# Optimization experiments

Measured on AMD Instinct MI355X. Metric: run time of the kernel, lower is better.

## Reference

```python
import jax, jax.numpy as jnp
import numpy as np

D_MODEL = 1024
N_HEADS = 16
D_K = D_MODEL // N_HEADS


def setup_inputs() -> dict:
    key = jax.random.key(0)
    ks = jax.random.split(key, 11)
    B, S = 4, 2048
    scale = 1.0 / np.sqrt(D_MODEL)
    inp = {
        "Q": jax.random.normal(ks[0], (B, S, D_MODEL), jnp.float32),
        "K": jax.random.normal(ks[1], (B, S, D_MODEL), jnp.float32),
        "V": jax.random.normal(ks[2], (B, S, D_MODEL), jnp.float32),
        "Wq": jax.random.normal(ks[3], (D_MODEL, D_MODEL), jnp.float32) * scale,
        "bq": jnp.zeros((D_MODEL,), jnp.float32),
        "Wk": jax.random.normal(ks[4], (D_MODEL, D_MODEL), jnp.float32) * scale,
        "bk": jnp.zeros((D_MODEL,), jnp.float32),
        "Wv": jax.random.normal(ks[5], (D_MODEL, D_MODEL), jnp.float32) * scale,
        "bv": jnp.zeros((D_MODEL,), jnp.float32),
        "Wo": jax.random.normal(ks[6], (D_MODEL, D_MODEL), jnp.float32) * scale,
        "bo": jnp.zeros((D_MODEL,), jnp.float32),
    }
    return inp


def _split_heads(x):
    B, S, _ = x.shape
    return x.reshape(B, S, N_HEADS, D_K).transpose(0, 2, 1, 3)  # [B,H,S,Dk]


def reference(Q, K, V, Wq, bq, Wk, bk, Wv, bv, Wo, bo):
    # torch nn.Linear: y = x @ W.T + b
    q = _split_heads(Q @ Wq.T + bq)
    k = _split_heads(K @ Wk.T + bk)
    v = _split_heads(V @ Wv.T + bv)
    scores = jnp.einsum("bhsd,bhtd->bhst", q, k) / jnp.sqrt(jnp.float32(D_K))
    probs = jax.nn.softmax(scores, axis=-1)
    attn = jnp.einsum("bhst,bhtd->bhsd", probs, v)  # [B,H,S,Dk]
    B, H, S, Dk = attn.shape
    combined = attn.transpose(0, 2, 1, 3).reshape(B, S, H * Dk)
    return combined @ Wo.T + bo
```

## Files before the change

### kernel.cpp

```cpp
#include <hip/hip_runtime.h>
#include <hip/hip_bf16.h>

typedef float  f32x4  __attribute__((ext_vector_type(4)));
typedef float  f32x16 __attribute__((ext_vector_type(16)));
typedef float  fvec4  __attribute__((ext_vector_type(4)));
typedef __bf16 bf16x8 __attribute__((ext_vector_type(8)));
typedef unsigned short u16x4 __attribute__((ext_vector_type(4)));
typedef unsigned short u16x8 __attribute__((ext_vector_type(8)));
typedef unsigned int   u32x4 __attribute__((ext_vector_type(4)));

#define DEVINL __device__ __forceinline__

constexpr int D_MODEL = 1024;
constexpr int NH      = 16;
constexpr int DK      = 64;
constexpr int SEQ     = 2048;
constexpr int BATCH   = 4;
constexpr int M_TOK   = BATCH * SEQ;

DEVINL unsigned short f32_to_bf16_u(float f) {
    unsigned int u = __builtin_bit_cast(unsigned int, f);
    u = (u + 0x7FFFu + ((u >> 16) & 1u)) >> 16;
    return (unsigned short)u;
}

DEVINL float exp2_fast(float x) { return __builtin_amdgcn_exp2f(x); }
DEVINL float mx3(float a, float b, float c) { return fmaxf(fmaxf(a, b), c); }

DEVINL unsigned cvt_pk_bf16(float lo, float hi_) {
    unsigned d;
    asm("v_cvt_pk_bf16_f32 %0, %1, %2" : "=v"(d) : "v"(lo), "v"(hi_));
    return d;
}

DEVINL void gload_lds16(const void* g, void* l) {
    __builtin_amdgcn_global_load_lds(
        (const __attribute__((address_space(1))) void*)g,
        (__attribute__((address_space(3))) void*)l, 16, 0, 0);
}

DEVINL int vperm_s(int s0) { return (s0 & ~12) | ((s0 & 4) << 1) | ((s0 & 8) >> 1); }

__global__ __launch_bounds__(256) void cvt4(const float* __restrict__ a,
                                            const float* __restrict__ b,
                                            const float* __restrict__ c,
                                            const float* __restrict__ d,
                                            unsigned short* __restrict__ dst, int n8)
{
    int y = blockIdx.y;
    const float* s = (y == 0) ? a : (y == 1) ? b : (y == 2) ? c : d;
    size_t i = blockIdx.x * 256 + threadIdx.x;
    fvec4 v0 = *reinterpret_cast<const fvec4*>(s + i * 8);
    fvec4 v1 = *reinterpret_cast<const fvec4*>(s + i * 8 + 4);
    bf16x8 o;
    #pragma unroll
    for (int j = 0; j < 4; ++j) { o[j] = (__bf16)v0[j]; o[j + 4] = (__bf16)v1[j]; }
    *reinterpret_cast<bf16x8*>(dst + ((size_t)y * n8 + i) * 8) = o;
}

__global__ __launch_bounds__(256) void cvt3(const float* __restrict__ a,
                                            const float* __restrict__ b,
                                            const float* __restrict__ c,
                                            unsigned short* __restrict__ dst, int n8)
{
    int y = blockIdx.y;
    const float* s = (y == 0) ? a : (y == 1) ? b : c;
    size_t i = blockIdx.x * 256 + threadIdx.x;
    fvec4 v0 = *reinterpret_cast<const fvec4*>(s + i * 8);
    fvec4 v1 = *reinterpret_cast<const fvec4*>(s + i * 8 + 4);
    bf16x8 o;
    #pragma unroll
    for (int j = 0; j < 4; ++j) { o[j] = (__bf16)v0[j]; o[j + 4] = (__bf16)v1[j]; }
    *reinterpret_cast<bf16x8*>(dst + ((size_t)y * n8 + i) * 8) = o;
}

template<bool QKV>
__global__ __launch_bounds__(256) void gemm_bf(
    const unsigned short* __restrict__ A0, const unsigned short* __restrict__ W0,
    const float* __restrict__ B0, void* __restrict__ O0,
    const unsigned short* __restrict__ A1, const unsigned short* __restrict__ W1,
    const float* __restrict__ B1, void* __restrict__ O1,
    const unsigned short* __restrict__ A2, const unsigned short* __restrict__ W2,
    const float* __restrict__ B2, void* __restrict__ O2,
    float qscale)
{
    constexpr int K = D_MODEL, N = D_MODEL;
    __shared__ char As_[128 * 64 * 2];
    __shared__ char Bs_[128 * 64 * 2];

    const int y = QKV ? (int)blockIdx.y : 0;
    const unsigned short* Ap = (y == 0) ? A0 : (y == 1) ? A1 : A2;
    const unsigned short* Wb = (y == 0) ? W0 : (y == 1) ? W1 : W2;
    const float* bias = (y == 0) ? B0 : (y == 1) ? B1 : B2;

    const int tid  = threadIdx.x;
    const int lane = tid & 63;
    const int wave = tid >> 6;
    const int wr = (wave >> 1) * 64;
    const int wc = (wave & 1) * 64;
    const int wg = ((int)blockIdx.x & 7) * 64 + ((int)blockIdx.x >> 3);
    const int n0 = (wg & 7) * 128;
    const int m0 = (wg >> 3) * 128;
    const int l15 = lane & 15, h16 = lane >> 4;

    f32x4 acc[4][4] = {};

    for (int kt = 0; kt < K; kt += 64) {
        __syncthreads();
        #pragma unroll
        for (int i = 0; i < 4; ++i) {
            int chunk = tid + i * 256;
            int r = chunk >> 3, c16 = chunk & 7;
            int cs = (c16 ^ (r & 7)) * 8;
            gload_lds16(Wb + (size_t)(n0 + r) * K + kt + cs, Bs_ + chunk * 16);
            gload_lds16(Ap + (size_t)(m0 + r) * K + kt + cs, As_ + chunk * 16);
        }
        __syncthreads();

        #pragma unroll
        for (int kk = 0; kk < 2; ++kk) {
            bf16x8 af[4], bfr[4];
            #pragma unroll
            for (int mi = 0; mi < 4; ++mi) {
                int r = wr + mi * 16 + l15;
                af[mi] = *reinterpret_cast<const bf16x8*>(
                    As_ + ((r * 128 + kk * 64 + h16 * 16) ^ ((r & 7) << 4)));
            }
            #pragma unroll
            for (int ni = 0; ni < 4; ++ni) {
                int r = wc + ni * 16 + l15;
                bfr[ni] = *reinterpret_cast<const bf16x8*>(
                    Bs_ + ((r * 128 + kk * 64 + h16 * 16) ^ ((r & 7) << 4)));
            }
            #pragma unroll
            for (int mi = 0; mi < 4; ++mi)
                #pragma unroll
                for (int ni = 0; ni < 4; ++ni)
                    acc[mi][ni] = __builtin_amdgcn_mfma_f32_16x16x32_bf16(
                        af[mi], bfr[ni], acc[mi][ni], 0, 0, 0);
        }
    }

    const int rl = h16 * 4;
    #pragma unroll
    for (int mi = 0; mi < 4; ++mi) {
        #pragma unroll
        for (int ni = 0; ni < 4; ++ni) {
            int col = n0 + wc + ni * 16 + l15;
            float bv = bias[col];
            if constexpr (QKV) {
                float sc = (y == 0) ? qscale : 1.0f;
                if (y == 2) {
                    int row0 = m0 + wr + mi * 16 + rl;
                    int bb = row0 >> 11, s0 = row0 & (SEQ - 1);
                    int sp = vperm_s(s0);
                    int h = col >> 6, dk = col & (DK - 1);
                    u16x4 o;
                    #pragma unroll
                    for (int r = 0; r < 4; ++r)
                        o[r] = f32_to_bf16_u(acc[mi][ni][r] + bv);
                    *reinterpret_cast<u16x4*>((unsigned short*)O2 +
                        (((size_t)bb * NH + h) * DK + dk) * SEQ + sp) = o;
                } else {
                    unsigned short* op = (unsigned short*)((y == 0) ? O0 : O1);
                    #pragma unroll
                    for (int r = 0; r < 4; ++r) {
                        int row = m0 + wr + mi * 16 + rl + r;
                        int bb = row >> 11, s = row & (SEQ - 1);
                        int h = col >> 6, dk = col & (DK - 1);
                        op[((((size_t)bb * NH + h) * SEQ) + s) * DK + dk]
                            = f32_to_bf16_u((acc[mi][ni][r] + bv) * sc);
                    }
                }
            } else {
                #pragma unroll
                for (int r = 0; r < 4; ++r) {
                    int row = m0 + wr + mi * 16 + rl + r;
                    ((float*)O0)[(size_t)row * N + col] = acc[mi][ni][r] + bv;
                }
            }
        }
    }
}

template<int OMODE>
__global__ __launch_bounds__(256) void gemm_f32a(const float* __restrict__ Ap,
                                                 const unsigned short* __restrict__ Wb,
                                                 const float* __restrict__ bias,
                                                 void* __restrict__ outp,
                                                 float out_scale)
{
    constexpr int K = D_MODEL, N = D_MODEL;
    __shared__ char As_[128 * 64 * 2];
    __shared__ char Bs_[128 * 64 * 2];

    const int tid  = threadIdx.x;
    const int lane = tid & 63;
    const int wave = tid >> 6;
    const int wr = (wave >> 1) * 64;
    const int wc = (wave & 1) * 64;
    const int wg = ((int)blockIdx.x & 7) * 64 + ((int)blockIdx.x >> 3);
    const int n0 = (wg & 7) * 128;
    const int m0 = (wg >> 3) * 128;
    const int l15 = lane & 15, h16 = lane >> 4;

    f32x4 acc[4][4] = {};

    for (int kt = 0; kt < K; kt += 64) {
        __syncthreads();
        #pragma unroll
        for (int i = 0; i < 4; ++i) {
            int chunk = tid + i * 256;
            int r = chunk >> 3, c16 = chunk & 7;
            int cs = (c16 ^ (r & 7)) * 8;
            gload_lds16(Wb + (size_t)(n0 + r) * K + kt + cs, Bs_ + chunk * 16);
            const float* src = Ap + (size_t)(m0 + r) * K + kt + c16 * 8;
            fvec4 v0 = *reinterpret_cast<const fvec4*>(src);
            fvec4 v1 = *reinterpret_cast<const fvec4*>(src + 4);
            bf16x8 o;
            #pragma unroll
            for (int j = 0; j < 4; ++j) { o[j] = (__bf16)v0[j]; o[j + 4] = (__bf16)v1[j]; }
            *reinterpret_cast<bf16x8*>(As_ + ((chunk * 16) ^ ((r & 7) << 4))) = o;
        }
        __syncthreads();

        #pragma unroll
        for (int kk = 0; kk < 2; ++kk) {
            bf16x8 af[4], bfr[4];
            #pragma unroll
            for (int mi = 0; mi < 4; ++mi) {
                int r = wr + mi * 16 + l15;
                af[mi] = *reinterpret_cast<const bf16x8*>(
                    As_ + ((r * 128 + kk * 64 + h16 * 16) ^ ((r & 7) << 4)));
            }
            #pragma unroll
            for (int ni = 0; ni < 4; ++ni) {
                int r = wc + ni * 16 + l15;
                bfr[ni] = *reinterpret_cast<const bf16x8*>(
                    Bs_ + ((r * 128 + kk * 64 + h16 * 16) ^ ((r & 7) << 4)));
            }
            #pragma unroll
            for (int mi = 0; mi < 4; ++mi)
                #pragma unroll
                for (int ni = 0; ni < 4; ++ni)
                    acc[mi][ni] = __builtin_amdgcn_mfma_f32_16x16x32_bf16(
                        af[mi], bfr[ni], acc[mi][ni], 0, 0, 0);
        }
    }

    const int rl = h16 * 4;
    #pragma unroll
    for (int mi = 0; mi < 4; ++mi) {
        #pragma unroll
        for (int ni = 0; ni < 4; ++ni) {
            int col = n0 + wc + ni * 16 + l15;
            float bv = bias[col];
            if constexpr (OMODE == 2) {
                int row0 = m0 + wr + mi * 16 + rl;
                int bb = row0 >> 11, s0 = row0 & (SEQ - 1);
                int sp = vperm_s(s0);
                int h = col >> 6, dk = col & (DK - 1);
                u16x4 o;
                #pragma unroll
                for (int r = 0; r < 4; ++r)
                    o[r] = f32_to_bf16_u((acc[mi][ni][r] + bv) * out_scale);
                *reinterpret_cast<u16x4*>((unsigned short*)outp +
                    (((size_t)bb * NH + h) * DK + dk) * SEQ + sp) = o;
            } else {
                #pragma unroll
                for (int r = 0; r < 4; ++r) {
                    int row = m0 + wr + mi * 16 + rl + r;
                    int bb = row >> 11, s = row & (SEQ - 1);
                    int h = col >> 6, dk = col & (DK - 1);
                    ((unsigned short*)outp)[((((size_t)bb * NH + h) * SEQ) + s) * DK + dk]
                        = f32_to_bf16_u((acc[mi][ni][r] + bv) * out_scale);
                }
            }
        }
    }
}

__global__ __launch_bounds__(512, 4) void attn_kernel(const unsigned short* __restrict__ qb,
                                                      const unsigned short* __restrict__ kb,
                                                      const unsigned short* __restrict__ vt,
                                                      unsigned short* __restrict__ ob)
{
    constexpr float THR = 11.0f;
    __shared__ char lds[32768];

    const int tid  = threadIdx.x;
    const int lane = tid & 63;
    const int tl31 = lane & 31;
    const int hi   = lane >> 5;
    const int wave = tid >> 6;
    const int wg   = ((int)blockIdx.x & 7) * 64 + ((int)blockIdx.x >> 3);
    const int bh   = wg >> 3;
    const int q0   = (wg & 7) * 256;
    const size_t base  = (size_t)bh * SEQ * DK;
    const size_t baseT = (size_t)bh * DK * SEQ;

    const int k_kt = tid >> 8, k_kd = (tid >> 6) & 3, k_hi = (tid >> 5) & 1, k_tl = tid & 31;
    const size_t k_goff = base + (size_t)(k_kt * 32 + k_tl) * DK + k_kd * 16 + k_hi * 8;
    const int v_tg = tid >> 6, v_dh = (tid >> 5) & 1, v_dl = tid & 31;
    const size_t v_goff = baseT + (size_t)(v_dh * 32 + v_dl) * SEQ + v_tg * 8;

    bf16x8 qf[4];
    #pragma unroll
    for (int kd = 0; kd < 4; ++kd)
        qf[kd] = *reinterpret_cast<const bf16x8*>(
            qb + base + (size_t)(q0 + wave * 32 + tl31) * DK + kd * 16 + hi * 8);

    f32x16 oaccT[2] = {};
    float m_run = -1e30f, l_run = 0.f;

    {
        u16x8 kreg = *reinterpret_cast<const u16x8*>(kb + k_goff);
        u16x8 vreg = *reinterpret_cast<const u16x8*>(vt + v_goff);
        *reinterpret_cast<u16x8*>(lds + tid * 16) = kreg;
        *reinterpret_cast<u16x8*>(lds + 8192 + tid * 16) = vreg;
    }
    __syncthreads();

    for (int t = 0; t < 32; ++t) {
        const int cur = t & 1;
        const char* Kr = lds + cur * 16384;
        const char* Vr = Kr + 8192;

        u16x8 kreg, vreg;
        if (t < 31) {
            const int t0n = (t + 1) * 64;
            kreg = *reinterpret_cast<const u16x8*>(kb + k_goff + (size_t)t0n * DK);
            vreg = *reinterpret_cast<const u16x8*>(vt + v_goff + t0n);
        }

        f32x16 sT[2] = {};
        #pragma unroll
        for (int kt = 0; kt < 2; ++kt)
            #pragma unroll
            for (int kd = 0; kd < 4; ++kd) {
                bf16x8 kf = *reinterpret_cast<const bf16x8*>(Kr + kt * 4096 + kd * 1024 + lane * 16);
                sT[kt] = __builtin_amdgcn_mfma_f32_32x32x16_bf16(kf, qf[kd], sT[kt], 0, 0, 0);
            }

        float m;
        {
            float tm[2];
            #pragma unroll
            for (int kt = 0; kt < 2; ++kt) {
                float g0 = mx3(sT[kt][0],  sT[kt][1],  sT[kt][2]);
                float g1 = mx3(sT[kt][3],  sT[kt][4],  sT[kt][5]);
                float g2 = mx3(sT[kt][6],  sT[kt][7],  sT[kt][8]);
                float g3 = mx3(sT[kt][9],  sT[kt][10], sT[kt][11]);
                float g4 = mx3(sT[kt][12], sT[kt][13], sT[kt][14]);
                tm[kt] = fmaxf(mx3(g0, g1, g2), mx3(g3, g4, sT[kt][15]));
            }
            m = fmaxf(tm[0], tm[1]);
            m = fmaxf(m, __shfl_xor(m, 32));
        }
        if (__any(m > m_run + THR)) {
            float mn = fmaxf(m_run, m);
            float al = exp2_fast(m_run - mn);
            m_run = mn;
            l_run *= al;
            oaccT[0] *= al;
            oaccT[1] *= al;
        }
        {
            float rs0 = 0.f, rs1 = 0.f, rs2 = 0.f, rs3 = 0.f;
            #pragma unroll
            for (int kt = 0; kt < 2; ++kt)
                #pragma unroll
                for (int i = 0; i < 16; i += 4) {
                    float p0 = exp2_fast(sT[kt][i + 0] - m_run);
                    float p1 = exp2_fast(sT[kt][i + 1] - m_run);
                    float p2 = exp2_fast(sT[kt][i + 2] - m_run);
                    float p3 = exp2_fast(sT[kt][i + 3] - m_run);
                    sT[kt][i + 0] = p0; sT[kt][i + 1] = p1;
                    sT[kt][i + 2] = p2; sT[kt][i + 3] = p3;
                    rs0 += p0; rs1 += p1; rs2 += p2; rs3 += p3;
                }
            float rs = (rs0 + rs1) + (rs2 + rs3);
            rs += __shfl_xor(rs, 32);
            l_run += rs;
        }

        #pragma unroll
        for (int ks = 0; ks < 4; ++ks) {
            bf16x8 vfA0 = *reinterpret_cast<const bf16x8*>(Vr + ks * 2048 + hi * 1024 + tl31 * 16);
            bf16x8 vfA1 = *reinterpret_cast<const bf16x8*>(Vr + ks * 2048 + hi * 1024 + 512 + tl31 * 16);
            const int kt = ks >> 1, r0 = (ks & 1) * 8;
            u32x4 w;
            w[0] = cvt_pk_bf16(sT[kt][r0 + 0], sT[kt][r0 + 1]);
            w[1] = cvt_pk_bf16(sT[kt][r0 + 2], sT[kt][r0 + 3]);
            w[2] = cvt_pk_bf16(sT[kt][r0 + 4], sT[kt][r0 + 5]);
            w[3] = cvt_pk_bf16(sT[kt][r0 + 6], sT[kt][r0 + 7]);
            bf16x8 pa = __builtin_bit_cast(bf16x8, w);
            oaccT[0] = __builtin_amdgcn_mfma_f32_32x32x16_bf16(vfA0, pa, oaccT[0], 0, 0, 0);
            oaccT[1] = __builtin_amdgcn_mfma_f32_32x32x16_bf16(vfA1, pa, oaccT[1], 0, 0, 0);
        }

        if (t < 31) {
            char* Kw = lds + (cur ^ 1) * 16384;
            *reinterpret_cast<u16x8*>(Kw + tid * 16) = kreg;
            *reinterpret_cast<u16x8*>(Kw + 8192 + tid * 16) = vreg;
        }
        __syncthreads();
    }

    char* myregion = lds + wave * 4096;
    const int bb = bh >> 4, h = bh & 15;
    {
        float rl = 1.0f / l_run;
        #pragma unroll
        for (int dh = 0; dh < 2; ++dh)
            #pragma unroll
            for (int r = 0; r < 16; ++r) {
                int dl = (r & 3) + 8 * (r >> 2) + 4 * hi + 32 * dh;
                int boff = (tl31 * 128 + dl * 2) ^ ((tl31 & 7) << 4);
                *reinterpret_cast<unsigned short*>(myregion + boff) =
                    f32_to_bf16_u(oaccT[dh][r] * rl);
            }
        #pragma unroll
        for (int c = 0; c < 4; ++c) {
            int chunk = lane + c * 64;
            int row = chunk >> 3, c16 = chunk & 7;
            int boff = (row * 128 + c16 * 16) ^ ((row & 7) << 4);
            u16x8 v = *reinterpret_cast<const u16x8*>(myregion + boff);
            size_t tok = (size_t)(bb * SEQ) + q0 + wave * 32 + row;
            *reinterpret_cast<u16x8*>(ob + tok * D_MODEL + h * DK + c16 * 8) = v;
        }
    }
}

extern "C" void kernel_launch(void* const* d_in, const int* in_sizes, int n_in,
                              void* d_out, int out_size, void* d_ws, size_t ws_size,
                              hipStream_t stream)
{
    const float* Q  = (const float*)d_in[0];
    const float* K_ = (const float*)d_in[1];
    const float* V  = (const float*)d_in[2];
    const float* Wq = (const float*)d_in[3];
    const float* bq = (const float*)d_in[4];
    const float* Wk = (const float*)d_in[5];
    const float* bk = (const float*)d_in[6];
    const float* Wv = (const float*)d_in[7];
    const float* bv = (const float*)d_in[8];
    const float* Wo = (const float*)d_in[9];
    const float* bo = (const float*)d_in[10];
    float* out = (float*)d_out;

    const size_t SZ = (size_t)M_TOK * D_MODEL;
    const size_t WZ = (size_t)D_MODEL * D_MODEL;
    unsigned short* qh_ = (unsigned short*)d_ws;
    unsigned short* kh_ = qh_ + SZ;
    unsigned short* vh_ = kh_ + SZ;
    unsigned short* ah_ = vh_ + SZ;
    unsigned short* wqb = ah_ + SZ;
    unsigned short* wkb = wqb + WZ;
    unsigned short* wvb = wkb + WZ;
    unsigned short* wob = wvb + WZ;
    unsigned short* qbf = wob + WZ;
    unsigned short* kbf = qbf + SZ;
    unsigned short* vbf = kbf + SZ;

    const bool big = ws_size >= (size_t)(4 * SZ + 4 * WZ + 3 * SZ) * 2;
    const float qscale = 0.125f * 1.4426950408889634f;

    cvt4<<<dim3((int)(WZ / 8 / 256), 4), 256, 0, stream>>>(Wq, Wk, Wv, Wo, wqb, (int)(WZ / 8));

    if (big) {
        cvt3<<<dim3((int)(SZ / 8 / 256), 3), 256, 0, stream>>>(Q, K_, V, qbf, (int)(SZ / 8));
        gemm_bf<true><<<dim3(512, 3), 256, 0, stream>>>(
            qbf, wqb, bq, qh_,  kbf, wkb, bk, kh_,  vbf, wvb, bv, vh_, qscale);
    } else {
        gemm_f32a<1><<<512, 256, 0, stream>>>(Q,  wqb, bq, qh_, qscale);
        gemm_f32a<1><<<512, 256, 0, stream>>>(K_, wkb, bk, kh_, 1.0f);
        gemm_f32a<2><<<512, 256, 0, stream>>>(V,  wvb, bv, vh_, 1.0f);
    }
    attn_kernel<<<512, 512, 0, stream>>>(qh_, kh_, vh_, ah_);
    gemm_bf<false><<<dim3(512, 1), 256, 0, stream>>>(
        ah_, wob, bo, out,  nullptr, nullptr, nullptr, nullptr,
        nullptr, nullptr, nullptr, nullptr, 1.0f);
}
```

Measured before the change: 203.7 us.

## Drop input bf16 pre-conversion path and add MFMA priority hints in attention

Measured after the change: 203.6 us. Within noise of the previous version (-0.1%).

```diff
diff --git a/kernel.cpp b/kernel.cpp
--- a/kernel.cpp
+++ b/kernel.cpp
@@ -58,131 +58,6 @@
     *reinterpret_cast<bf16x8*>(dst + ((size_t)y * n8 + i) * 8) = o;
 }
 
-__global__ __launch_bounds__(256) void cvt3(const float* __restrict__ a,
-                                            const float* __restrict__ b,
-                                            const float* __restrict__ c,
-                                            unsigned short* __restrict__ dst, int n8)
-{
-    int y = blockIdx.y;
-    const float* s = (y == 0) ? a : (y == 1) ? b : c;
-    size_t i = blockIdx.x * 256 + threadIdx.x;
-    fvec4 v0 = *reinterpret_cast<const fvec4*>(s + i * 8);
-    fvec4 v1 = *reinterpret_cast<const fvec4*>(s + i * 8 + 4);
-    bf16x8 o;
-    #pragma unroll
-    for (int j = 0; j < 4; ++j) { o[j] = (__bf16)v0[j]; o[j + 4] = (__bf16)v1[j]; }
-    *reinterpret_cast<bf16x8*>(dst + ((size_t)y * n8 + i) * 8) = o;
-}
-
-template<bool QKV>
-__global__ __launch_bounds__(256) void gemm_bf(
-    const unsigned short* __restrict__ A0, const unsigned short* __restrict__ W0,
-    const float* __restrict__ B0, void* __restrict__ O0,
-    const unsigned short* __restrict__ A1, const unsigned short* __restrict__ W1,
-    const float* __restrict__ B1, void* __restrict__ O1,
-    const unsigned short* __restrict__ A2, const unsigned short* __restrict__ W2,
-    const float* __restrict__ B2, void* __restrict__ O2,
-    float qscale)
-{
-    constexpr int K = D_MODEL, N = D_MODEL;
-    __shared__ char As_[128 * 64 * 2];
-    __shared__ char Bs_[128 * 64 * 2];
-
-    const int y = QKV ? (int)blockIdx.y : 0;
-    const unsigned short* Ap = (y == 0) ? A0 : (y == 1) ? A1 : A2;
-    const unsigned short* Wb = (y == 0) ? W0 : (y == 1) ? W1 : W2;
-    const float* bias = (y == 0) ? B0 : (y == 1) ? B1 : B2;
-
-    const int tid  = threadIdx.x;
-    const int lane = tid & 63;
-    const int wave = tid >> 6;
-    const int wr = (wave >> 1) * 64;
-    const int wc = (wave & 1) * 64;
-    const int wg = ((int)blockIdx.x & 7) * 64 + ((int)blockIdx.x >> 3);
-    const int n0 = (wg & 7) * 128;
-    const int m0 = (wg >> 3) * 128;
-    const int l15 = lane & 15, h16 = lane >> 4;
-
-    f32x4 acc[4][4] = {};
-
-    for (int kt = 0; kt < K; kt += 64) {
-        __syncthreads();
-        #pragma unroll
-        for (int i = 0; i < 4; ++i) {
-            int chunk = tid + i * 256;
-            int r = chunk >> 3, c16 = chunk & 7;
-            int cs = (c16 ^ (r & 7)) * 8;
-            gload_lds16(Wb + (size_t)(n0 + r) * K + kt + cs, Bs_ + chunk * 16);
-            gload_lds16(Ap + (size_t)(m0 + r) * K + kt + cs, As_ + chunk * 16);
-        }
-        __syncthreads();
-
-        #pragma unroll
-        for (int kk = 0; kk < 2; ++kk) {
-            bf16x8 af[4], bfr[4];
-            #pragma unroll
-            for (int mi = 0; mi < 4; ++mi) {
-                int r = wr + mi * 16 + l15;
-                af[mi] = *reinterpret_cast<const bf16x8*>(
-                    As_ + ((r * 128 + kk * 64 + h16 * 16) ^ ((r & 7) << 4)));
-            }
-            #pragma unroll
-            for (int ni = 0; ni < 4; ++ni) {
-                int r = wc + ni * 16 + l15;
-                bfr[ni] = *reinterpret_cast<const bf16x8*>(
-                    Bs_ + ((r * 128 + kk * 64 + h16 * 16) ^ ((r & 7) << 4)));
-            }
-            #pragma unroll
-            for (int mi = 0; mi < 4; ++mi)
-                #pragma unroll
-                for (int ni = 0; ni < 4; ++ni)
-                    acc[mi][ni] = __builtin_amdgcn_mfma_f32_16x16x32_bf16(
-                        af[mi], bfr[ni], acc[mi][ni], 0, 0, 0);
-        }
-    }
-
-    const int rl = h16 * 4;
-    #pragma unroll
-    for (int mi = 0; mi < 4; ++mi) {
-        #pragma unroll
-        for (int ni = 0; ni < 4; ++ni) {
-            int col = n0 + wc + ni * 16 + l15;
-            float bv = bias[col];
-            if constexpr (QKV) {
-                float sc = (y == 0) ? qscale : 1.0f;
-                if (y == 2) {
-                    int row0 = m0 + wr + mi * 16 + rl;
-                    int bb = row0 >> 11, s0 = row0 & (SEQ - 1);
-                    int sp = vperm_s(s0);
-                    int h = col >> 6, dk = col & (DK - 1);
-                    u16x4 o;
-                    #pragma unroll
-                    for (int r = 0; r < 4; ++r)
-                        o[r] = f32_to_bf16_u(acc[mi][ni][r] + bv);
-                    *reinterpret_cast<u16x4*>((unsigned short*)O2 +
-                        (((size_t)bb * NH + h) * DK + dk) * SEQ + sp) = o;
-                } else {
-                    unsigned short* op = (unsigned short*)((y == 0) ? O0 : O1);
-                    #pragma unroll
-                    for (int r = 0; r < 4; ++r) {
-                        int row = m0 + wr + mi * 16 + rl + r;
-                        int bb = row >> 11, s = row & (SEQ - 1);
-                        int h = col >> 6, dk = col & (DK - 1);
-                        op[((((size_t)bb * NH + h) * SEQ) + s) * DK + dk]
-                            = f32_to_bf16_u((acc[mi][ni][r] + bv) * sc);
-                    }
-                }
-            } else {
-                #pragma unroll
-                for (int r = 0; r < 4; ++r) {
-                    int row = m0 + wr + mi * 16 + rl + r;
-                    ((float*)O0)[(size_t)row * N + col] = acc[mi][ni][r] + bv;
-                }
-            }
-        }
-    }
-}
-
 template<int OMODE>
 __global__ __launch_bounds__(256) void gemm_f32a(const float* __restrict__ Ap,
                                                  const unsigned short* __restrict__ Wb,
@@ -190,7 +65,7 @@
                                                  void* __restrict__ outp,
                                                  float out_scale)
 {
-    constexpr int K = D_MODEL, N = D_MODEL;
+    constexpr int K = D_MODEL;
     __shared__ char As_[128 * 64 * 2];
     __shared__ char Bs_[128 * 64 * 2];
 
@@ -280,6 +155,79 @@
     }
 }
 
+__global__ __launch_bounds__(256) void gemm_obf(const unsigned short* __restrict__ Ap,
+                                                const unsigned short* __restrict__ Wb,
+                                                const float* __restrict__ bias,
+                                                float* __restrict__ outp)
+{
+    constexpr int K = D_MODEL, N = D_MODEL;
+    __shared__ char As_[128 * 64 * 2];
+    __shared__ char Bs_[128 * 64 * 2];
+
+    const int tid  = threadIdx.x;
+    const int lane = tid & 63;
+    const int wave = tid >> 6;
+    const int wr = (wave >> 1) * 64;
+    const int wc = (wave & 1) * 64;
+    const int wg = ((int)blockIdx.x & 7) * 64 + ((int)blockIdx.x >> 3);
+    const int n0 = (wg & 7) * 128;
+    const int m0 = (wg >> 3) * 128;
+    const int l15 = lane & 15, h16 = lane >> 4;
+
+    f32x4 acc[4][4] = {};
+
+    for (int kt = 0; kt < K; kt += 64) {
+        __syncthreads();
+        #pragma unroll
+        for (int i = 0; i < 4; ++i) {
+            int chunk = tid + i * 256;
+            int r = chunk >> 3, c16 = chunk & 7;
+            int cs = (c16 ^ (r & 7)) * 8;
+            gload_lds16(Wb + (size_t)(n0 + r) * K + kt + cs, Bs_ + chunk * 16);
+            gload_lds16(Ap + (size_t)(m0 + r) * K + kt + cs, As_ + chunk * 16);
+        }
+        __syncthreads();
+
+        #pragma unroll
+        for (int kk = 0; kk < 2; ++kk) {
+            bf16x8 af[4], bfr[4];
+            #pragma unroll
+            for (int mi = 0; mi < 4; ++mi) {
+                int r = wr + mi * 16 + l15;
+                af[mi] = *reinterpret_cast<const bf16x8*>(
+                    As_ + ((r * 128 + kk * 64 + h16 * 16) ^ ((r & 7) << 4)));
+            }
+            #pragma unroll
+            for (int ni = 0; ni < 4; ++ni) {
+                int r = wc + ni * 16 + l15;
+                bfr[ni] = *reinterpret_cast<const bf16x8*>(
+                    Bs_ + ((r * 128 + kk * 64 + h16 * 16) ^ ((r & 7) << 4)));
+            }
+            #pragma unroll
+            for (int mi = 0; mi < 4; ++mi)
+                #pragma unroll
+                for (int ni = 0; ni < 4; ++ni)
+                    acc[mi][ni] = __builtin_amdgcn_mfma_f32_16x16x32_bf16(
+                        af[mi], bfr[ni], acc[mi][ni], 0, 0, 0);
+        }
+    }
+
+    const int rl = h16 * 4;
+    #pragma unroll
+    for (int mi = 0; mi < 4; ++mi) {
+        #pragma unroll
+        for (int ni = 0; ni < 4; ++ni) {
+            int col = n0 + wc + ni * 16 + l15;
+            float bv = bias[col];
+            #pragma unroll
+            for (int r = 0; r < 4; ++r) {
+                int row = m0 + wr + mi * 16 + rl + r;
+                outp[(size_t)row * N + col] = acc[mi][ni][r] + bv;
+            }
+        }
+    }
+}
+
 __global__ __launch_bounds__(512, 4) void attn_kernel(const unsigned short* __restrict__ qb,
                                                       const unsigned short* __restrict__ kb,
                                                       const unsigned short* __restrict__ vt,
@@ -334,6 +282,7 @@
         }
 
         f32x16 sT[2] = {};
+        __builtin_amdgcn_s_setprio(1);
         #pragma unroll
         for (int kt = 0; kt < 2; ++kt)
             #pragma unroll
@@ -341,6 +290,7 @@
                 bf16x8 kf = *reinterpret_cast<const bf16x8*>(Kr + kt * 4096 + kd * 1024 + lane * 16);
                 sT[kt] = __builtin_amdgcn_mfma_f32_32x32x16_bf16(kf, qf[kd], sT[kt], 0, 0, 0);
             }
+        __builtin_amdgcn_s_setprio(0);
 
         float m;
         {
@@ -384,6 +334,7 @@
             l_run += rs;
         }
 
+        __builtin_amdgcn_s_setprio(1);
         #pragma unroll
         for (int ks = 0; ks < 4; ++ks) {
             bf16x8 vfA0 = *reinterpret_cast<const bf16x8*>(Vr + ks * 2048 + hi * 1024 + tl31 * 16);
@@ -398,6 +349,7 @@
             oaccT[0] = __builtin_amdgcn_mfma_f32_32x32x16_bf16(vfA0, pa, oaccT[0], 0, 0, 0);
             oaccT[1] = __builtin_amdgcn_mfma_f32_32x32x16_bf16(vfA1, pa, oaccT[1], 0, 0, 0);
         }
+        __builtin_amdgcn_s_setprio(0);
 
         if (t < 31) {
             char* Kw = lds + (cur ^ 1) * 16384;
@@ -459,26 +411,14 @@
     unsigned short* wkb = wqb + WZ;
     unsigned short* wvb = wkb + WZ;
     unsigned short* wob = wvb + WZ;
-    unsigned short* qbf = wob + WZ;
-    unsigned short* kbf = qbf + SZ;
-    unsigned short* vbf = kbf + SZ;
-
-    const bool big = ws_size >= (size_t)(4 * SZ + 4 * WZ + 3 * SZ) * 2;
+
     const float qscale = 0.125f * 1.4426950408889634f;
 
     cvt4<<<dim3((int)(WZ / 8 / 256), 4), 256, 0, stream>>>(Wq, Wk, Wv, Wo, wqb, (int)(WZ / 8));
 
-    if (big) {
-        cvt3<<<dim3((int)(SZ / 8 / 256), 3), 256, 0, stream>>>(Q, K_, V, qbf, (int)(SZ / 8));
-        gemm_bf<true><<<dim3(512, 3), 256, 0, stream>>>(
-            qbf, wqb, bq, qh_,  kbf, wkb, bk, kh_,  vbf, wvb, bv, vh_, qscale);
-    } else {
-        gemm_f32a<1><<<512, 256, 0, stream>>>(Q,  wqb, bq, qh_, qscale);
-        gemm_f32a<1><<<512, 256, 0, stream>>>(K_, wkb, bk, kh_, 1.0f);
-        gemm_f32a<2><<<512, 256, 0, stream>>>(V,  wvb, bv, vh_, 1.0f);
-    }
+    gemm_f32a<1><<<512, 256, 0, stream>>>(Q,  wqb, bq, qh_, qscale);
+    gemm_f32a<1><<<512, 256, 0, stream>>>(K_, wkb, bk, kh_, 1.0f);
+    gemm_f32a<2><<<512, 256, 0, stream>>>(V,  wvb, bv, vh_, 1.0f);
     attn_kernel<<<512, 512, 0, stream>>>(qh_, kh_, vh_, ah_);
-    gemm_bf<false><<<dim3(512, 1), 256, 0, stream>>>(
-        ah_, wob, bo, out,  nullptr, nullptr, nullptr, nullptr,
-        nullptr, nullptr, nullptr, nullptr, 1.0f);
-}
+    gemm_obf<<<512, 256, 0, stream>>>(ah_, wob, bo, out);
+}
```
